# Kernel optimization log

Measured on AMD Instinct MI355X. Metric: run time of the kernel, lower is better.

## Reference

```python
import jax, jax.numpy as jnp
import numpy as np

# CMSBlockLinear block-ELL sparse linear forward.
# values: [R, K, B, B] active weight tiles (out_tile x in_tile)
# col_indices: [R, K] int32, which input block-column each tile multiplies
# y[b,s, r*B+i] = sum_k sum_j values[r,k,i,j] * x[b,s, col_indices[r,k]*B + j] + bias

IN_FEATURES = 2048
OUT_FEATURES = 2048
TILE = 16
DENSITY = 0.25
R = OUT_FEATURES // TILE   # 128
C = IN_FEATURES // TILE    # 128
K = max(1, int(C * DENSITY))  # 32
BATCH, SEQ = 4, 512


def setup_inputs() -> dict:
    key = jax.random.key(0)
    kx, kv, kc = jax.random.split(key, 3)
    x = jax.random.normal(kx, (BATCH, SEQ, IN_FEATURES), dtype=jnp.float32)
    # Kaiming-normal init as in _reset_parameters: std = gain('relu') / sqrt(K*B)
    std = np.sqrt(2.0) / np.sqrt(K * TILE)
    values = jax.random.normal(kv, (R, K, TILE, TILE), dtype=jnp.float32) * std
    # K distinct column indices per row (random topology, as in _initialize_topology)
    rng = np.random.default_rng(0)
    col_np = np.stack([rng.permutation(C)[:K] for _ in range(R)]).astype(np.int32)
    col_indices = jnp.asarray(col_np)
    bias = jnp.zeros((OUT_FEATURES,), dtype=jnp.float32)
    return {"x": x, "values": values, "col_indices": col_indices, "bias": bias}


def reference(x, values, col_indices, bias):
    bs, sl, _ = x.shape
    Rr, Kk, B, _ = values.shape
    Cc = x.shape[-1] // B
    x_blocks = x.reshape(bs, sl, Cc, B)                 # [b, s, C, B]
    # Gather the K active input blocks for every output row: [b, s, R, K, B]
    x_gathered = x_blocks[:, :, col_indices, :]
    # Batched small-block matmul and reduce over K tiles: [b, s, R, B]
    out = jnp.einsum("bsrkj,rkij->bsri", x_gathered, values)
    return out.reshape(bs, sl, Rr * B) + bias
```

## Files before the change

### kernel.cpp

```cpp
#include <hip/hip_runtime.h>
#include <hip/hip_bf16.h>

#define TOKS 2048
#define FEAT 2048
#define NR   128
#define KB   32
#define RB   32
#define TT   32

typedef __attribute__((ext_vector_type(8))) short bf16x8;
typedef __attribute__((ext_vector_type(4))) float f32x4;

__device__ __forceinline__ unsigned short f2bf(float f) {
    unsigned u = __builtin_bit_cast(unsigned, f);
    u += 0x7FFFu + ((u >> 16) & 1u);
    return (unsigned short)(u >> 16);
}

__device__ __forceinline__ bf16x8 pack8(float4 a, float4 b) {
    bf16x8 r;
    r[0] = (short)f2bf(a.x); r[1] = (short)f2bf(a.y);
    r[2] = (short)f2bf(a.z); r[3] = (short)f2bf(a.w);
    r[4] = (short)f2bf(b.x); r[5] = (short)f2bf(b.y);
    r[6] = (short)f2bf(b.z); r[7] = (short)f2bf(b.w);
    return r;
}

__global__ __launch_bounds__(256) void cvt_values_kernel(const float* __restrict__ v,
                                                         unsigned short* __restrict__ o,
                                                         int n) {
    int i = (blockIdx.x * 256 + threadIdx.x) * 4;
    if (i + 3 < n) {
        float4 f = *reinterpret_cast<const float4*>(v + i);
        ushort4 r;
        r.x = f2bf(f.x); r.y = f2bf(f.y); r.z = f2bf(f.z); r.w = f2bf(f.w);
        *reinterpret_cast<ushort4*>(o + i) = r;
    }
}

template<bool VB16>
__device__ __forceinline__ void load_frags(const void* __restrict__ values,
                                           const int* __restrict__ cols,
                                           int r, int q, int n, int h,
                                           int mrow, int axor,
                                           bf16x8* bfrag, int* aaddr) {
    int cbase = __builtin_amdgcn_readfirstlane(r) * KB;
    if (VB16) {
        const unsigned short* vbl = reinterpret_cast<const unsigned short*>(values)
            + ((size_t)r << 13) + (q << 8) + (n << 4) + (h << 3);
        #pragma unroll
        for (int t = 0; t < 16; ++t) {
            bfrag[t] = *reinterpret_cast<const bf16x8*>(vbl + t * 512);
            int c = cols[cbase + 2 * t + q];
            aaddr[t] = mrow + (((c << 5) + (h << 4)) ^ axor);
        }
    } else {
        const float* vfl = reinterpret_cast<const float*>(values)
            + ((size_t)r << 13) + (q << 8) + (n << 4) + (h << 3);
        #pragma unroll
        for (int t = 0; t < 16; ++t) {
            const float4* pv = reinterpret_cast<const float4*>(vfl + t * 512);
            bfrag[t] = pack8(pv[0], pv[1]);
            int c = cols[cbase + 2 * t + q];
            aaddr[t] = mrow + (((c << 5) + (h << 4)) ^ axor);
        }
    }
}

template<bool VB16>
__global__ __launch_bounds__(1024, 4) void bsp_kernel(const float* __restrict__ x,
                                                      const void* __restrict__ values,
                                                      const int* __restrict__ cols,
                                                      const float* __restrict__ bias,
                                                      float* __restrict__ out) {
    __shared__ __align__(16) unsigned short xs[TT * FEAT];

    int bid  = blockIdx.x;
    int xcd  = bid & 7, slot = bid >> 3;
    int tg   = xcd * 8 + (slot >> 2);
    int rg   = slot & 3;
    int tok0 = tg * TT;
    int r0   = rg * RB;
    int tid  = threadIdx.x;

    {
        int tr = tid >> 8;
        int ch = tid & 255;
        #pragma unroll 2
        for (int it = 0; it < 8; ++it) {
            int t = it * 4 + tr;
            const float4* p = reinterpret_cast<const float4*>(
                x + (size_t)(tok0 + t) * FEAT + ch * 8);
            float4 a = p[0], b = p[1];
            int off = (t << 12) + ((ch << 4) ^ ((t & 7) << 4));
            *reinterpret_cast<bf16x8*>(reinterpret_cast<char*>(xs) + off) = pack8(a, b);
        }
    }

    int wave = tid >> 6;
    int lane = tid & 63;
    int n = lane & 15;
    int g = lane >> 4;
    int h = g & 1;
    int q = g >> 1;

    int mrow = n << 12;
    int axor = (n & 7) << 4;

    bf16x8 bfrag[16];
    int aaddr[16];
    load_frags<VB16>(values, cols, r0 + wave * 2, q, n, h, mrow, axor, bfrag, aaddr);

    __syncthreads();

    #pragma unroll 1
    for (int rr = 0; rr < 2; ++rr) {
        int r = r0 + wave * 2 + rr;
        if (rr > 0)
            load_frags<VB16>(values, cols, r, q, n, h, mrow, axor, bfrag, aaddr);

        float fb = bias[(r << 4) + n];

        #pragma unroll
        for (int sx = 0; sx < 2; ++sx) {
            const char* xb = reinterpret_cast<const char*>(xs) + (sx << 16);
            f32x4 acc0 = {0.f, 0.f, 0.f, 0.f};
            f32x4 acc1 = {0.f, 0.f, 0.f, 0.f};
            #pragma unroll
            for (int t = 0; t < 8; ++t) {
                bf16x8 a0 = *reinterpret_cast<const bf16x8*>(xb + aaddr[2 * t]);
                bf16x8 a1 = *reinterpret_cast<const bf16x8*>(xb + aaddr[2 * t + 1]);
                acc0 = __builtin_amdgcn_mfma_f32_16x16x32_bf16(a0, bfrag[2 * t],     acc0, 0, 0, 0);
                acc1 = __builtin_amdgcn_mfma_f32_16x16x32_bf16(a1, bfrag[2 * t + 1], acc1, 0, 0, 0);
            }
            int trow = tok0 + (sx << 4) + (g << 2);
            size_t ob = (size_t)trow * 2048 + (r << 4) + n;
            #pragma unroll
            for (int p = 0; p < 4; ++p)
                out[ob + (size_t)p * 2048] = acc0[p] + acc1[p] + fb;
        }
    }
}

extern "C" void kernel_launch(void* const* d_in, const int* in_sizes, int n_in,
                              void* d_out, int out_size, void* d_ws, size_t ws_size,
                              hipStream_t stream) {
    const float* x      = (const float*)d_in[0];
    const float* values = (const float*)d_in[1];
    const int*   cols   = (const int*)d_in[2];
    const float* bias   = (const float*)d_in[3];
    float*       out    = (float*)d_out;

    const int nv = NR * KB * 16 * 16;
    const int grid = (TOKS / TT) * (NR / RB);

    if (ws_size >= (size_t)nv * sizeof(unsigned short)) {
        unsigned short* vb = (unsigned short*)d_ws;
        cvt_values_kernel<<<nv / (256 * 4), 256, 0, stream>>>(values, vb, nv);
        bsp_kernel<true><<<grid, 1024, 0, stream>>>(x, vb, cols, bias, out);
    } else {
        bsp_kernel<false><<<grid, 1024, 0, stream>>>(x, values, cols, bias, out);
    }
}
```

Baseline: 24.34 us.

## Pre-convert x to bf16 in a prep kernel and stage via global_load_lds

A single prep kernel now converts both x and the weight values to bf16 in workspace. The main kernel then copies the bf16 token rows straight into LDS with global_load_lds, using a lane-swizzled source address in place of the per-thread convert-and-store path. This is meant to remove the fp32-to-bf16 packing work and VGPR traffic from the main kernel's staging phase. In exchange it adds a full 16 MB read and 8 MB write of x in the prep pass, which may cost more than it saves, and it depends on the workspace being large enough.

Result: slower. 25.26 us (+3.8%).

```diff
diff --git a/kernel.cpp b/kernel.cpp
--- a/kernel.cpp
+++ b/kernel.cpp
@@ -26,53 +26,118 @@
     return r;
 }
 
-__global__ __launch_bounds__(256) void cvt_values_kernel(const float* __restrict__ v,
-                                                         unsigned short* __restrict__ o,
-                                                         int n) {
-    int i = (blockIdx.x * 256 + threadIdx.x) * 4;
-    if (i + 3 < n) {
-        float4 f = *reinterpret_cast<const float4*>(v + i);
-        ushort4 r;
-        r.x = f2bf(f.x); r.y = f2bf(f.y); r.z = f2bf(f.z); r.w = f2bf(f.w);
-        *reinterpret_cast<ushort4*>(o + i) = r;
-    }
-}
-
-template<bool VB16>
-__device__ __forceinline__ void load_frags(const void* __restrict__ values,
-                                           const int* __restrict__ cols,
-                                           int r, int q, int n, int h,
-                                           int mrow, int axor,
-                                           bf16x8* bfrag, int* aaddr) {
-    int cbase = __builtin_amdgcn_readfirstlane(r) * KB;
-    if (VB16) {
-        const unsigned short* vbl = reinterpret_cast<const unsigned short*>(values)
-            + ((size_t)r << 13) + (q << 8) + (n << 4) + (h << 3);
+__global__ __launch_bounds__(256) void prep_kernel(const float* __restrict__ x,
+                                                   const float* __restrict__ v,
+                                                   unsigned short* __restrict__ xb,
+                                                   unsigned short* __restrict__ vb) {
+    int bid = blockIdx.x;
+    const float* src;
+    unsigned short* dst;
+    size_t base;
+    if (bid < 2048) { src = x; dst = xb; base = ((size_t)bid * 256 + threadIdx.x) * 8; }
+    else            { src = v; dst = vb; base = ((size_t)(bid - 2048) * 256 + threadIdx.x) * 8; }
+    float4 a = *reinterpret_cast<const float4*>(src + base);
+    float4 b = *reinterpret_cast<const float4*>(src + base + 4);
+    *reinterpret_cast<bf16x8*>(dst + base) = pack8(a, b);
+}
+
+__global__ __launch_bounds__(1024) void bsp3(const unsigned short* __restrict__ xb,
+                                             const unsigned short* __restrict__ vb,
+                                             const int* __restrict__ cols,
+                                             const float* __restrict__ bias,
+                                             float* __restrict__ out) {
+    __shared__ __align__(16) unsigned short xs[TT * FEAT];
+
+    int bid  = blockIdx.x;
+    int xcd  = bid & 7, slot = bid >> 3;
+    int tg   = xcd * 8 + (slot >> 2);
+    int rg   = slot & 3;
+    int tok0 = tg * TT;
+    int r0   = rg * RB;
+    int tid  = threadIdx.x;
+    int wave = tid >> 6;
+    int lane = tid & 63;
+
+    #pragma unroll
+    for (int i = 0; i < 2; ++i) {
+        int t = wave * 2 + i;
+        const unsigned short* rowp = xb + (size_t)(tok0 + t) * FEAT;
+        int lsw = lane ^ (t & 7);
+        #pragma unroll
+        for (int s = 0; s < 4; ++s) {
+            __builtin_amdgcn_global_load_lds(
+                (const __attribute__((address_space(1))) void*)(rowp + (s * 64 + lsw) * 8),
+                (__attribute__((address_space(3))) void*)(xs + t * 2048 + s * 512),
+                16, 0, 0);
+        }
+    }
+
+    int n = lane & 15;
+    int g = lane >> 4;
+    int h = g & 1;
+    int q = g >> 1;
+
+    int mrow = n << 12;
+    int axor = (n & 7) << 4;
+
+    bf16x8 bfrag[16];
+    int aaddr[16];
+    {
+        int r = r0 + wave * 2;
+        int cbase = __builtin_amdgcn_readfirstlane(r) * KB;
+        const unsigned short* vbl = vb + ((size_t)r << 13) + (q << 8) + (n << 4) + (h << 3);
         #pragma unroll
         for (int t = 0; t < 16; ++t) {
             bfrag[t] = *reinterpret_cast<const bf16x8*>(vbl + t * 512);
             int c = cols[cbase + 2 * t + q];
             aaddr[t] = mrow + (((c << 5) + (h << 4)) ^ axor);
         }
-    } else {
-        const float* vfl = reinterpret_cast<const float*>(values)
-            + ((size_t)r << 13) + (q << 8) + (n << 4) + (h << 3);
-        #pragma unroll
-        for (int t = 0; t < 16; ++t) {
-            const float4* pv = reinterpret_cast<const float4*>(vfl + t * 512);
-            bfrag[t] = pack8(pv[0], pv[1]);
-            int c = cols[cbase + 2 * t + q];
-            aaddr[t] = mrow + (((c << 5) + (h << 4)) ^ axor);
-        }
-    }
-}
-
-template<bool VB16>
-__global__ __launch_bounds__(1024, 4) void bsp_kernel(const float* __restrict__ x,
-                                                      const void* __restrict__ values,
-                                                      const int* __restrict__ cols,
-                                                      const float* __restrict__ bias,
-                                                      float* __restrict__ out) {
+    }
+
+    __syncthreads();
+
+    #pragma unroll 1
+    for (int rr = 0; rr < 2; ++rr) {
+        int r = r0 + wave * 2 + rr;
+        if (rr > 0) {
+            int cbase = __builtin_amdgcn_readfirstlane(r) * KB;
+            const unsigned short* vbl = vb + ((size_t)r << 13) + (q << 8) + (n << 4) + (h << 3);
+            #pragma unroll
+            for (int t = 0; t < 16; ++t) {
+                bfrag[t] = *reinterpret_cast<const bf16x8*>(vbl + t * 512);
+                int c = cols[cbase + 2 * t + q];
+                aaddr[t] = mrow + (((c << 5) + (h << 4)) ^ axor);
+            }
+        }
+
+        float fb = bias[(r << 4) + n];
+
+        #pragma unroll
+        for (int sx = 0; sx < 2; ++sx) {
+            const char* xbp = reinterpret_cast<const char*>(xs) + (sx << 16);
+            f32x4 acc0 = {0.f, 0.f, 0.f, 0.f};
+            f32x4 acc1 = {0.f, 0.f, 0.f, 0.f};
+            #pragma unroll
+            for (int t = 0; t < 8; ++t) {
+                bf16x8 a0 = *reinterpret_cast<const bf16x8*>(xbp + aaddr[2 * t]);
+                bf16x8 a1 = *reinterpret_cast<const bf16x8*>(xbp + aaddr[2 * t + 1]);
+                acc0 = __builtin_amdgcn_mfma_f32_16x16x32_bf16(a0, bfrag[2 * t],     acc0, 0, 0, 0);
+                acc1 = __builtin_amdgcn_mfma_f32_16x16x32_bf16(a1, bfrag[2 * t + 1], acc1, 0, 0, 0);
+            }
+            int trow = tok0 + (sx << 4) + (g << 2);
+            size_t ob = (size_t)trow * 2048 + (r << 4) + n;
+            #pragma unroll
+            for (int p = 0; p < 4; ++p)
+                out[ob + (size_t)p * 2048] = acc0[p] + acc1[p] + fb;
+        }
+    }
+}
+
+__global__ __launch_bounds__(1024, 4) void bsp_fb(const float* __restrict__ x,
+                                                  const float* __restrict__ values,
+                                                  const int* __restrict__ cols,
+                                                  const float* __restrict__ bias,
+                                                  float* __restrict__ out) {
     __shared__ __align__(16) unsigned short xs[TT * FEAT];
 
     int bid  = blockIdx.x;
@@ -96,6 +161,7 @@
             *reinterpret_cast<bf16x8*>(reinterpret_cast<char*>(xs) + off) = pack8(a, b);
         }
     }
+    __syncthreads();
 
     int wave = tid >> 6;
     int lane = tid & 63;
@@ -103,33 +169,33 @@
     int g = lane >> 4;
     int h = g & 1;
     int q = g >> 1;
-
     int mrow = n << 12;
     int axor = (n & 7) << 4;
-
-    bf16x8 bfrag[16];
-    int aaddr[16];
-    load_frags<VB16>(values, cols, r0 + wave * 2, q, n, h, mrow, axor, bfrag, aaddr);
-
-    __syncthreads();
 
     #pragma unroll 1
     for (int rr = 0; rr < 2; ++rr) {
         int r = r0 + wave * 2 + rr;
-        if (rr > 0)
-            load_frags<VB16>(values, cols, r, q, n, h, mrow, axor, bfrag, aaddr);
-
+        int cbase = __builtin_amdgcn_readfirstlane(r) * KB;
+        bf16x8 bfrag[16];
+        int aaddr[16];
+        const float* vfl = values + ((size_t)r << 13) + (q << 8) + (n << 4) + (h << 3);
+        #pragma unroll
+        for (int t = 0; t < 16; ++t) {
+            const float4* pv = reinterpret_cast<const float4*>(vfl + t * 512);
+            bfrag[t] = pack8(pv[0], pv[1]);
+            int c = cols[cbase + 2 * t + q];
+            aaddr[t] = mrow + (((c << 5) + (h << 4)) ^ axor);
+        }
         float fb = bias[(r << 4) + n];
-
         #pragma unroll
         for (int sx = 0; sx < 2; ++sx) {
-            const char* xb = reinterpret_cast<const char*>(xs) + (sx << 16);
+            const char* xbp = reinterpret_cast<const char*>(xs) + (sx << 16);
             f32x4 acc0 = {0.f, 0.f, 0.f, 0.f};
             f32x4 acc1 = {0.f, 0.f, 0.f, 0.f};
             #pragma unroll
             for (int t = 0; t < 8; ++t) {
-                bf16x8 a0 = *reinterpret_cast<const bf16x8*>(xb + aaddr[2 * t]);
-                bf16x8 a1 = *reinterpret_cast<const bf16x8*>(xb + aaddr[2 * t + 1]);
+                bf16x8 a0 = *reinterpret_cast<const bf16x8*>(xbp + aaddr[2 * t]);
+                bf16x8 a1 = *reinterpret_cast<const bf16x8*>(xbp + aaddr[2 * t + 1]);
                 acc0 = __builtin_amdgcn_mfma_f32_16x16x32_bf16(a0, bfrag[2 * t],     acc0, 0, 0, 0);
                 acc1 = __builtin_amdgcn_mfma_f32_16x16x32_bf16(a1, bfrag[2 * t + 1], acc1, 0, 0, 0);
             }
@@ -151,14 +217,16 @@
     const float* bias   = (const float*)d_in[3];
     float*       out    = (float*)d_out;
 
-    const int nv = NR * KB * 16 * 16;
+    const size_t xb_bytes = (size_t)TOKS * FEAT * 2;
+    const size_t vb_bytes = (size_t)NR * KB * 256 * 2;
     const int grid = (TOKS / TT) * (NR / RB);
 
-    if (ws_size >= (size_t)nv * sizeof(unsigned short)) {
-        unsigned short* vb = (unsigned short*)d_ws;
-        cvt_values_kernel<<<nv / (256 * 4), 256, 0, stream>>>(values, vb, nv);
-        bsp_kernel<true><<<grid, 1024, 0, stream>>>(x, vb, cols, bias, out);
+    if (ws_size >= xb_bytes + vb_bytes) {
+        unsigned short* xbuf = (unsigned short*)d_ws;
+        unsigned short* vbuf = (unsigned short*)((char*)d_ws + xb_bytes);
+        prep_kernel<<<2048 + 512, 256, 0, stream>>>(x, values, xbuf, vbuf);
+        bsp3<<<grid, 1024, 0, stream>>>(xbuf, vbuf, cols, bias, out);
     } else {
-        bsp_kernel<false><<<grid, 1024, 0, stream>>>(x, values, cols, bias, out);
-    }
-}
+        bsp_fb<<<grid, 1024, 0, stream>>>(x, values, cols, bias, out);
+    }
+}
```

## Halve block threads, give each wave four rows and overlap x staging with compute

Applied to the files above, without the earlier changes.

The main kernel now runs with 512 threads per block, and each wave handles four output row tiles instead of two. The x tile is staged in two token halves. The second half is kept in registers and written to shared memory while the first half's MFMAs run, and weight fragments for two rows are loaded before the barrier. The goal is to overlap global-load latency and shared-memory writes with compute and to reuse each staged x tile across more rows. The cost is much higher register pressure (two sets of 16 fragments plus staged x values), which may lower occupancy or cause spills.

New measurement: 25.19 us. 1.03x slower.

```diff
diff --git a/kernel.cpp b/kernel.cpp
--- a/kernel.cpp
+++ b/kernel.cpp
@@ -38,41 +38,152 @@
     }
 }
 
-template<bool VB16>
-__device__ __forceinline__ void load_frags(const void* __restrict__ values,
-                                           const int* __restrict__ cols,
-                                           int r, int q, int n, int h,
-                                           int mrow, int axor,
-                                           bf16x8* bfrag, int* aaddr) {
-    int cbase = __builtin_amdgcn_readfirstlane(r) * KB;
-    if (VB16) {
-        const unsigned short* vbl = reinterpret_cast<const unsigned short*>(values)
-            + ((size_t)r << 13) + (q << 8) + (n << 4) + (h << 3);
-        #pragma unroll
-        for (int t = 0; t < 16; ++t) {
-            bfrag[t] = *reinterpret_cast<const bf16x8*>(vbl + t * 512);
-            int c = cols[cbase + 2 * t + q];
-            aaddr[t] = mrow + (((c << 5) + (h << 4)) ^ axor);
-        }
-    } else {
-        const float* vfl = reinterpret_cast<const float*>(values)
-            + ((size_t)r << 13) + (q << 8) + (n << 4) + (h << 3);
-        #pragma unroll
-        for (int t = 0; t < 16; ++t) {
-            const float4* pv = reinterpret_cast<const float4*>(vfl + t * 512);
-            bfrag[t] = pack8(pv[0], pv[1]);
-            int c = cols[cbase + 2 * t + q];
-            aaddr[t] = mrow + (((c << 5) + (h << 4)) ^ axor);
-        }
-    }
-}
-
-template<bool VB16>
-__global__ __launch_bounds__(1024, 4) void bsp_kernel(const float* __restrict__ x,
-                                                      const void* __restrict__ values,
-                                                      const int* __restrict__ cols,
-                                                      const float* __restrict__ bias,
-                                                      float* __restrict__ out) {
+__device__ __forceinline__ void load_r_frags(const unsigned short* __restrict__ vb,
+                                             const int* __restrict__ cols,
+                                             int r, int q, int n, int h,
+                                             int mrow, int axor,
+                                             bf16x8* bf, int* aa) {
+    int cb = __builtin_amdgcn_readfirstlane(r) * KB;
+    const unsigned short* vbl = vb + ((size_t)r << 13) + (q << 8) + (n << 4) + (h << 3);
+    #pragma unroll
+    for (int t = 0; t < 16; ++t) {
+        bf[t] = *reinterpret_cast<const bf16x8*>(vbl + t * 512);
+        int c0 = cols[cb + 2 * t];
+        int c1 = cols[cb + 2 * t + 1];
+        int c  = q ? c1 : c0;
+        aa[t] = mrow + (((c << 5) + (h << 4)) ^ axor);
+    }
+}
+
+__device__ __forceinline__ f32x4 dot_r(const char* __restrict__ xbp,
+                                       const int* aa, const bf16x8* bf) {
+    f32x4 a0 = {0.f, 0.f, 0.f, 0.f};
+    f32x4 a1 = {0.f, 0.f, 0.f, 0.f};
+    #pragma unroll
+    for (int t = 0; t < 8; ++t) {
+        bf16x8 x0 = *reinterpret_cast<const bf16x8*>(xbp + aa[2 * t]);
+        bf16x8 x1 = *reinterpret_cast<const bf16x8*>(xbp + aa[2 * t + 1]);
+        a0 = __builtin_amdgcn_mfma_f32_16x16x32_bf16(x0, bf[2 * t],     a0, 0, 0, 0);
+        a1 = __builtin_amdgcn_mfma_f32_16x16x32_bf16(x1, bf[2 * t + 1], a1, 0, 0, 0);
+    }
+    return a0 + a1;
+}
+
+__device__ __forceinline__ void store_r(float* __restrict__ out, int tok0, int sx,
+                                        int g, int r, int n, float fb, f32x4 acc) {
+    int trow = tok0 + (sx << 4) + (g << 2);
+    size_t ob = (size_t)trow * 2048 + (r << 4) + n;
+    #pragma unroll
+    for (int p = 0; p < 4; ++p)
+        out[ob + (size_t)p * 2048] = acc[p] + fb;
+}
+
+__global__ __launch_bounds__(512) void bsp4(const float* __restrict__ x,
+                                            const unsigned short* __restrict__ vb,
+                                            const int* __restrict__ cols,
+                                            const float* __restrict__ bias,
+                                            float* __restrict__ out) {
+    __shared__ __align__(16) unsigned short xs[TT * FEAT];
+
+    int bid  = blockIdx.x;
+    int xcd  = bid & 7, slot = bid >> 3;
+    int tg   = xcd * 8 + (slot >> 2);
+    int rg   = slot & 3;
+    int tok0 = tg * TT;
+    int r0   = rg * RB;
+    int tid  = threadIdx.x;
+    int wave = tid >> 6;
+    int lane = tid & 63;
+
+    int tr = tid >> 8;
+    int ch = tid & 255;
+
+    float4 A0[8], B0[8];
+    #pragma unroll
+    for (int it = 0; it < 8; ++it) {
+        const float4* p = reinterpret_cast<const float4*>(
+            x + (size_t)(tok0 + it * 2 + tr) * FEAT + ch * 8);
+        A0[it] = p[0]; B0[it] = p[1];
+    }
+    float4 A1[8], B1[8];
+    #pragma unroll
+    for (int it = 0; it < 8; ++it) {
+        const float4* p = reinterpret_cast<const float4*>(
+            x + (size_t)(tok0 + 16 + it * 2 + tr) * FEAT + ch * 8);
+        A1[it] = p[0]; B1[it] = p[1];
+    }
+
+    #pragma unroll
+    for (int it = 0; it < 8; ++it) {
+        int t = it * 2 + tr;
+        int off = (t << 12) + ((ch << 4) ^ ((t & 7) << 4));
+        *reinterpret_cast<bf16x8*>(reinterpret_cast<char*>(xs) + off) = pack8(A0[it], B0[it]);
+    }
+    bf16x8 H1[8];
+    #pragma unroll
+    for (int it = 0; it < 8; ++it) H1[it] = pack8(A1[it], B1[it]);
+
+    int n = lane & 15;
+    int g = lane >> 4;
+    int h = g & 1;
+    int q = g >> 1;
+    int mrow = n << 12;
+    int axor = (n & 7) << 4;
+
+    int rA = r0 + wave * 4;
+    bf16x8 bfA[16], bfB[16];
+    int aaA[16], aaB[16];
+    load_r_frags(vb, cols, rA,     q, n, h, mrow, axor, bfA, aaA);
+    load_r_frags(vb, cols, rA + 1, q, n, h, mrow, axor, bfB, aaB);
+    float fbA = bias[(rA << 4) + n];
+    float fbB = bias[((rA + 1) << 4) + n];
+
+    __syncthreads();
+
+    #pragma unroll
+    for (int it = 0; it < 8; ++it) {
+        int t = it * 2 + tr + 16;
+        int off = (t << 12) + ((ch << 4) ^ ((t & 7) << 4));
+        *reinterpret_cast<bf16x8*>(reinterpret_cast<char*>(xs) + off) = H1[it];
+    }
+
+    const char* xb0 = reinterpret_cast<const char*>(xs);
+    f32x4 sA0 = dot_r(xb0, aaA, bfA);
+    f32x4 sB0 = dot_r(xb0, aaB, bfB);
+
+    __syncthreads();
+
+    const char* xb1 = reinterpret_cast<const char*>(xs) + 65536;
+    f32x4 sA1 = dot_r(xb1, aaA, bfA);
+    f32x4 sB1 = dot_r(xb1, aaB, bfB);
+
+    store_r(out, tok0, 0, g, rA,     n, fbA, sA0);
+    store_r(out, tok0, 1, g, rA,     n, fbA, sA1);
+    store_r(out, tok0, 0, g, rA + 1, n, fbB, sB0);
+    store_r(out, tok0, 1, g, rA + 1, n, fbB, sB1);
+
+    int rC = rA + 2;
+    load_r_frags(vb, cols, rC,     q, n, h, mrow, axor, bfA, aaA);
+    load_r_frags(vb, cols, rC + 1, q, n, h, mrow, axor, bfB, aaB);
+    float fbC = bias[(rC << 4) + n];
+    float fbD = bias[((rC + 1) << 4) + n];
+
+    f32x4 sC0 = dot_r(xb0, aaA, bfA);
+    f32x4 sD0 = dot_r(xb0, aaB, bfB);
+    f32x4 sC1 = dot_r(xb1, aaA, bfA);
+    f32x4 sD1 = dot_r(xb1, aaB, bfB);
+
+    store_r(out, tok0, 0, g, rC,     n, fbC, sC0);
+    store_r(out, tok0, 1, g, rC,     n, fbC, sC1);
+    store_r(out, tok0, 0, g, rC + 1, n, fbD, sD0);
+    store_r(out, tok0, 1, g, rC + 1, n, fbD, sD1);
+}
+
+__global__ __launch_bounds__(1024, 4) void bsp_fb(const float* __restrict__ x,
+                                                  const float* __restrict__ values,
+                                                  const int* __restrict__ cols,
+                                                  const float* __restrict__ bias,
+                                                  float* __restrict__ out) {
     __shared__ __align__(16) unsigned short xs[TT * FEAT];
 
     int bid  = blockIdx.x;
@@ -96,6 +207,7 @@
             *reinterpret_cast<bf16x8*>(reinterpret_cast<char*>(xs) + off) = pack8(a, b);
         }
     }
+    __syncthreads();
 
     int wave = tid >> 6;
     int lane = tid & 63;
@@ -103,33 +215,33 @@
     int g = lane >> 4;
     int h = g & 1;
     int q = g >> 1;
-
     int mrow = n << 12;
     int axor = (n & 7) << 4;
-
-    bf16x8 bfrag[16];
-    int aaddr[16];
-    load_frags<VB16>(values, cols, r0 + wave * 2, q, n, h, mrow, axor, bfrag, aaddr);
-
-    __syncthreads();
 
     #pragma unroll 1
     for (int rr = 0; rr < 2; ++rr) {
         int r = r0 + wave * 2 + rr;
-        if (rr > 0)
-            load_frags<VB16>(values, cols, r, q, n, h, mrow, axor, bfrag, aaddr);
-
+        int cbase = __builtin_amdgcn_readfirstlane(r) * KB;
+        bf16x8 bfrag[16];
+        int aaddr[16];
+        const float* vfl = values + ((size_t)r << 13) + (q << 8) + (n << 4) + (h << 3);
+        #pragma unroll
+        for (int t = 0; t < 16; ++t) {
+            const float4* pv = reinterpret_cast<const float4*>(vfl + t * 512);
+            bfrag[t] = pack8(pv[0], pv[1]);
+            int c = cols[cbase + 2 * t + q];
+            aaddr[t] = mrow + (((c << 5) + (h << 4)) ^ axor);
+        }
         float fb = bias[(r << 4) + n];
-
         #pragma unroll
         for (int sx = 0; sx < 2; ++sx) {
-            const char* xb = reinterpret_cast<const char*>(xs) + (sx << 16);
+            const char* xbp = reinterpret_cast<const char*>(xs) + (sx << 16);
             f32x4 acc0 = {0.f, 0.f, 0.f, 0.f};
             f32x4 acc1 = {0.f, 0.f, 0.f, 0.f};
             #pragma unroll
             for (int t = 0; t < 8; ++t) {
-                bf16x8 a0 = *reinterpret_cast<const bf16x8*>(xb + aaddr[2 * t]);
-                bf16x8 a1 = *reinterpret_cast<const bf16x8*>(xb + aaddr[2 * t + 1]);
+                bf16x8 a0 = *reinterpret_cast<const bf16x8*>(xbp + aaddr[2 * t]);
+                bf16x8 a1 = *reinterpret_cast<const bf16x8*>(xbp + aaddr[2 * t + 1]);
                 acc0 = __builtin_amdgcn_mfma_f32_16x16x32_bf16(a0, bfrag[2 * t],     acc0, 0, 0, 0);
                 acc1 = __builtin_amdgcn_mfma_f32_16x16x32_bf16(a1, bfrag[2 * t + 1], acc1, 0, 0, 0);
             }
@@ -155,10 +267,10 @@
     const int grid = (TOKS / TT) * (NR / RB);
 
     if (ws_size >= (size_t)nv * sizeof(unsigned short)) {
-        unsigned short* vb = (unsigned short*)d_ws;
-        cvt_values_kernel<<<nv / (256 * 4), 256, 0, stream>>>(values, vb, nv);
-        bsp_kernel<true><<<grid, 1024, 0, stream>>>(x, vb, cols, bias, out);
+        unsigned short* vbuf = (unsigned short*)d_ws;
+        cvt_values_kernel<<<nv / (256 * 4), 256, 0, stream>>>(values, vbuf, nv);
+        bsp4<<<grid, 512, 0, stream>>>(x, vbuf, cols, bias, out);
     } else {
-        bsp_kernel<false><<<grid, 1024, 0, stream>>>(x, values, cols, bias, out);
-    }
-}
+        bsp_fb<<<grid, 1024, 0, stream>>>(x, values, cols, bias, out);
+    }
+}
```
